# Performance work log

Hardware: AMD Instinct MI355X
Metric: run time of the kernel (lower is better)

The kernel has to match this reference:

```python
import jax, jax.numpy as jnp
import numpy as np
from jax import lax

CLIP = 5.0
LN_EPS = 1e-5


def _embed(feats, mean, std, W, b, g, beta):
    # InputNorm (eval mode, count>1): normalize with running stats, clamp.
    h = jnp.clip((feats - mean) / std, -CLIP, CLIP)
    h = lax.stop_gradient(h)  # torch runs InputNorm under no_grad
    # Linear + ReLU
    h = jax.nn.relu(h @ W + b)
    # LayerNorm over d_model
    mu = h.mean(-1, keepdims=True)
    var = ((h - mu) ** 2).mean(-1, keepdims=True)
    return (h - mu) / jnp.sqrt(var + LN_EPS) * g + beta


def setup_inputs() -> dict:
    key = jax.random.key(0)
    ks = jax.random.split(key, 8)
    nA, fA = 300000, 32
    nB, fB = 150000, 48
    d = 256
    B = 512
    inp = {
        "featsA": jax.random.normal(ks[0], (nA, fA), jnp.float32),
        "featsB": jax.random.normal(ks[1], (nB, fB), jnp.float32),
        "normA_mean": jnp.zeros((fA,), jnp.float32),
        "normA_std": jnp.ones((fA,), jnp.float32),
        "normB_mean": jnp.zeros((fB,), jnp.float32),
        "normB_std": jnp.ones((fB,), jnp.float32),
        "WA": jax.random.normal(ks[2], (fA, d), jnp.float32) / np.sqrt(fA),
        "bA": jnp.zeros((d,), jnp.float32),
        "lnA_g": jnp.ones((d,), jnp.float32),
        "lnA_b": jnp.zeros((d,), jnp.float32),
        "WB_": jax.random.normal(ks[3], (fB, d), jnp.float32) / np.sqrt(fB),
        "bB": jnp.zeros((d,), jnp.float32),
        "lnB_g": jnp.ones((d,), jnp.float32),
        "lnB_b": jnp.zeros((d,), jnp.float32),
        "Wback": jax.random.normal(ks[4], (d, d), jnp.float32) / np.sqrt(d),
        "bback": jnp.zeros((d,), jnp.float32),
        "Wv": jax.random.normal(ks[5], (d, 1), jnp.float32) / np.sqrt(d),
        "bv": jnp.zeros((1,), jnp.float32),
        "batch_index": jax.random.randint(ks[6], (nA + nB,), 0, B, jnp.int64)
        if jax.config.jax_enable_x64 else jax.random.randint(ks[6], (nA + nB,), 0, B, jnp.int32).astype(jnp.int32),
        "num_obs": B,
    }
    return inp


def reference(featsA, featsB, normA_mean, normA_std, normB_mean, normB_std,
              WA, bA, lnA_g, lnA_b, WB_, bB, lnB_g, lnB_b,
              Wback, bback, Wv, bv, batch_index, num_obs):
    # Per-entity-type embedding stacks, concatenated in entity-type order
    xA = _embed(featsA, normA_mean, normA_std, WA, bA, lnA_g, lnA_b)
    xB = _embed(featsB, normB_mean, normB_std, WB_, bB, lnB_g, lnB_b)
    x = jnp.concatenate([xA, xB], axis=0)          # [N, d]
    x = jax.nn.relu(x @ Wback + bback)              # backbone
    # torch_scatter mean pooling over observations
    sums = jax.ops.segment_sum(x, batch_index, num_segments=num_obs)
    counts = jax.ops.segment_sum(jnp.ones((x.shape[0],), x.dtype), batch_index,
                                 num_segments=num_obs)
    pooled = sums / jnp.maximum(counts, 1.0)[:, None]  # empty segments -> 0
    return pooled @ Wv + bv                          # [num_obs, 1]
```

## Files before the change

kernel.cpp:

```cpp
#include <hip/hip_runtime.h>

#define NSEG 512
#define NSPLIT 32

typedef __attribute__((ext_vector_type(8))) short short8;
typedef __attribute__((ext_vector_type(4))) short short4v;
typedef __attribute__((ext_vector_type(4))) float floatx4;

#define WS_WAT   0
#define WS_WBT2  16384
#define WS_W2GA  49152
#define WS_W2GB  180224
#define WS_C1A   311296
#define WS_C2A   312320
#define WS_C1B   313344
#define WS_C2B   314368
#define WS_INVA  315392
#define WS_INVB  315520
#define WS_VPART 315712
#define WS_CPART 381248

__device__ __forceinline__ short f2bf(float f) {
  unsigned u = __builtin_bit_cast(unsigned, f);
  u += 0x7FFFu + ((u >> 16) & 1u);
  return (short)(u >> 16);
}

__global__ void prep_kernel(const float* __restrict__ WA, const float* __restrict__ WB,
                            const float* __restrict__ Wback,
                            const float* __restrict__ gA, const float* __restrict__ betaA,
                            const float* __restrict__ gB, const float* __restrict__ betaB,
                            const float* __restrict__ bback,
                            const float* __restrict__ sA, const float* __restrict__ sB,
                            char* __restrict__ ws) {
  short* waT  = (short*)(ws + WS_WAT);
  short* wbT2 = (short*)(ws + WS_WBT2);
  short* w2gA = (short*)(ws + WS_W2GA);
  short* w2gB = (short*)(ws + WS_W2GB);
  float* c1A = (float*)(ws + WS_C1A);
  float* c2A = (float*)(ws + WS_C2A);
  float* c1B = (float*)(ws + WS_C1B);
  float* c2B = (float*)(ws + WS_C2B);
  float* invA = (float*)(ws + WS_INVA);
  float* invB = (float*)(ws + WS_INVB);
  float* vz   = (float*)(ws + WS_VPART);
  int tid = blockIdx.x * blockDim.x + threadIdx.x;
  int stride = gridDim.x * blockDim.x;
  for (int i = tid; i < 32*256; i += stride) {
    int n = i >> 5, k = i & 31;
    waT[i] = f2bf(WA[k*256 + n]);
  }
  for (int i = tid; i < 256*64; i += stride) {
    int n = i >> 6, k = i & 63;
    wbT2[i] = (k < 48) ? f2bf(WB[k*256 + n]) : (short)0;
  }
  for (int i = tid; i < 256*256; i += stride) {
    int n = i >> 8, k = i & 255;
    float w = Wback[k*256 + n];
    w2gA[i] = f2bf(gA[k] * w);
    w2gB[i] = f2bf(gB[k] * w);
  }
  if (blockIdx.x < 4 && threadIdx.x < 256) {
    int n = threadIdx.x;
    int which = blockIdx.x;
    const float* coef = (which == 0) ? gA : (which == 1) ? betaA : (which == 2) ? gB : betaB;
    float a = 0.f;
    #pragma unroll 8
    for (int k = 0; k < 256; k++) a = fmaf(coef[k], Wback[k*256 + n], a);
    if (which == 0)      c1A[n] = a;
    else if (which == 1) c2A[n] = a + bback[n];
    else if (which == 2) c1B[n] = a;
    else                 c2B[n] = a + bback[n];
  }
  if (tid < 32) invA[tid] = 1.0f / sA[tid];
  if (tid < 48) invB[tid] = 1.0f / sB[tid];
  for (int i = tid; i < 2*NSPLIT*NSEG; i += stride) vz[i] = 0.0f;
}

__global__ __launch_bounds__(256, 4) void fused_kernel(
    const float* __restrict__ featsA, const float* __restrict__ featsB,
    const float* __restrict__ mA, const float* __restrict__ mB,
    const float* __restrict__ bA, const float* __restrict__ bB,
    const float* __restrict__ Wv, const int* __restrict__ bidx,
    const char* __restrict__ ws, float* __restrict__ vpart, float* __restrict__ cpart,
    int tilesA, int nA, int nB)
{
  __shared__ __attribute__((aligned(16))) short ztile[64*264];
  __shared__ __attribute__((aligned(16))) float sred[64][4];
  __shared__ __attribute__((aligned(16))) float s2red[64][4];
  __shared__ __attribute__((aligned(16))) float vpw[64][4];

  const int tid  = threadIdx.x;
  const int wave = tid >> 6;
  const int lane = tid & 63;
  const int l15  = lane & 15;
  const int quad = lane >> 4;

  const bool isA = (blockIdx.x < (unsigned)tilesA);
  const int  tb  = isA ? blockIdx.x : (blockIdx.x - tilesA);
  const int  r0  = tb * 64;
  const int  nrows = isA ? nA : nB;
  const int  valid = min(64, nrows - r0);
  const float* feats = isA ? featsA : featsB;
  const float* meanp = isA ? mA : mB;
  const float* invp  = (const float*)(ws + (isA ? WS_INVA : WS_INVB));
  const float* biasp = isA ? bA : bB;
  const short* weT   = (const short*)(ws + (isA ? WS_WAT : WS_WBT2));
  const short* w2gT  = (const short*)(ws + (isA ? WS_W2GA : WS_W2GB));
  const float* c1p   = (const float*)(ws + (isA ? WS_C1A : WS_C1B));
  const float* c2p   = (const float*)(ws + (isA ? WS_C2A : WS_C2B));
  const int f       = isA ? 32 : 48;
  const int kstride = isA ? 32 : 64;
  const int ksteps  = isA ? 1 : 2;

  floatx4 acc1[4][4];
  #pragma unroll
  for (int mt = 0; mt < 4; mt++)
    #pragma unroll
    for (int nt = 0; nt < 4; nt++)
      acc1[mt][nt] = 0.0f;

  for (int kk = 0; kk < ksteps; kk++) {
    const int k0 = kk*32 + quad*8;
    const bool kvalid = (k0 < f);
    floatx4 mv0 = {0,0,0,0}, mv1 = {0,0,0,0}, iv0 = {1,1,1,1}, iv1 = {1,1,1,1};
    if (kvalid) {
      mv0 = *(const floatx4*)(meanp + k0);  mv1 = *(const floatx4*)(meanp + k0 + 4);
      iv0 = *(const floatx4*)(invp + k0);   iv1 = *(const floatx4*)(invp + k0 + 4);
    }
    short8 bfw[4];
    #pragma unroll
    for (int nt = 0; nt < 4; nt++)
      bfw[nt] = *(const short8*)(weT + (size_t)(64*wave + 16*nt + l15) * kstride + kk*32 + quad*8);
    #pragma unroll
    for (int mt = 0; mt < 4; mt++) {
      short8 a = {0,0,0,0,0,0,0,0};
      int row = 16*mt + l15;
      if (kvalid && row < valid) {
        const float* fp = feats + (size_t)(r0 + row) * f + k0;
        floatx4 x0 = *(const floatx4*)fp;
        floatx4 x1 = *(const floatx4*)(fp + 4);
        #pragma unroll
        for (int e = 0; e < 4; e++) {
          float h0 = (x0[e] - mv0[e]) * iv0[e];
          h0 = fminf(fmaxf(h0, -5.0f), 5.0f);
          a[e] = f2bf(h0);
          float h1 = (x1[e] - mv1[e]) * iv1[e];
          h1 = fminf(fmaxf(h1, -5.0f), 5.0f);
          a[4+e] = f2bf(h1);
        }
      }
      #pragma unroll
      for (int nt = 0; nt < 4; nt++)
        acc1[mt][nt] = __builtin_amdgcn_mfma_f32_16x16x32_bf16(bfw[nt], a, acc1[mt][nt], 0, 0, 0);
    }
  }

  float sacc[4], s2acc[4];
  #pragma unroll
  for (int mt = 0; mt < 4; mt++) { sacc[mt] = 0.f; s2acc[mt] = 0.f; }

  #pragma unroll
  for (int nt = 0; nt < 4; nt++) {
    const int c0 = 64*wave + 16*nt + 4*quad;
    floatx4 b1v = *(const floatx4*)(biasp + c0);
    #pragma unroll
    for (int mt = 0; mt < 4; mt++) {
      short4v pk;
      #pragma unroll
      for (int r = 0; r < 4; r++) {
        float h = fmaxf(acc1[mt][nt][r] + b1v[r], 0.0f);
        sacc[mt] += h;
        s2acc[mt] = fmaf(h, h, s2acc[mt]);
        pk[r] = f2bf(h);
      }
      *(short4v*)(ztile + (16*mt + l15)*264 + c0) = pk;
    }
  }
  #pragma unroll
  for (int mt = 0; mt < 4; mt++) {
    float s = sacc[mt], s2 = s2acc[mt];
    s += __shfl_xor(s, 16, 64);  s2 += __shfl_xor(s2, 16, 64);
    s += __shfl_xor(s, 32, 64);  s2 += __shfl_xor(s2, 32, 64);
    if (lane < 16) {
      sred[16*mt + lane][wave] = s;
      s2red[16*mt + lane][wave] = s2;
    }
  }
  __syncthreads();

  float rsv[4], mrsv[4];
  #pragma unroll
  for (int mt = 0; mt < 4; mt++) {
    int row = 16*mt + l15;
    floatx4 sv  = *(const floatx4*)sred[row];
    floatx4 s2v = *(const floatx4*)s2red[row];
    float s  = sv[0] + sv[1] + sv[2] + sv[3];
    float s2 = s2v[0] + s2v[1] + s2v[2] + s2v[3];
    float mu  = s * (1.0f/256.0f);
    float var = fmaxf(s2 * (1.0f/256.0f) - mu*mu, 0.0f);
    float rs  = rsqrtf(var + 1e-5f);
    rsv[mt]  = rs;
    mrsv[mt] = mu * rs;
  }

  floatx4 acc2[4][4];
  #pragma unroll
  for (int mt = 0; mt < 4; mt++)
    #pragma unroll
    for (int nt = 0; nt < 4; nt++)
      acc2[mt][nt] = 0.0f;

  #pragma unroll 2
  for (int kk = 0; kk < 8; kk++) {
    short8 bf[4];
    #pragma unroll
    for (int nt = 0; nt < 4; nt++)
      bf[nt] = *(const short8*)(w2gT + (size_t)(64*wave + 16*nt + l15)*256 + kk*32 + quad*8);
    #pragma unroll
    for (int mt = 0; mt < 4; mt++) {
      short8 a = *(const short8*)(ztile + (16*mt + l15)*264 + kk*32 + quad*8);
      #pragma unroll
      for (int nt = 0; nt < 4; nt++)
        acc2[mt][nt] = __builtin_amdgcn_mfma_f32_16x16x32_bf16(bf[nt], a, acc2[mt][nt], 0, 0, 0);
    }
  }

  float pv[4] = {0.f, 0.f, 0.f, 0.f};
  #pragma unroll
  for (int nt = 0; nt < 4; nt++) {
    const int c0 = 64*wave + 16*nt + 4*quad;
    floatx4 c1v = *(const floatx4*)(c1p + c0);
    floatx4 c2v = *(const floatx4*)(c2p + c0);
    floatx4 wvv = *(const floatx4*)(Wv + c0);
    #pragma unroll
    for (int mt = 0; mt < 4; mt++) {
      float rs = rsv[mt], mrs = mrsv[mt];
      #pragma unroll
      for (int r = 0; r < 4; r++) {
        float t = fmaf(-mrs, c1v[r], c2v[r]);
        float y = fmaf(rs, acc2[mt][nt][r], t);
        y = fmaxf(y, 0.0f);
        pv[mt] = fmaf(y, wvv[r], pv[mt]);
      }
    }
  }
  #pragma unroll
  for (int mt = 0; mt < 4; mt++) {
    float p = pv[mt];
    p += __shfl_xor(p, 16, 64);
    p += __shfl_xor(p, 32, 64);
    if (lane < 16) vpw[16*mt + lane][wave] = p;
  }
  __syncthreads();

  if (tid < valid) {
    floatx4 vv = *(const floatx4*)vpw[tid];
    float v = vv[0] + vv[1] + vv[2] + vv[3];
    int g = (isA ? r0 : (nA + r0)) + tid;
    int seg = bidx[g];
    int split = blockIdx.x & (NSPLIT - 1);
    atomicAdd(&vpart[split*NSEG + seg], v);
    atomicAdd(&cpart[split*NSEG + seg], 1.0f);
  }
}

__global__ void final_kernel(const float* __restrict__ vpart, const float* __restrict__ cpart,
                             const float* __restrict__ bv, float* __restrict__ out, int nseg) {
  int s = blockIdx.x * blockDim.x + threadIdx.x;
  if (s < nseg) {
    float a = 0.0f, c = 0.0f;
    #pragma unroll 8
    for (int i = 0; i < NSPLIT; i++) { a += vpart[i*NSEG + s]; c += cpart[i*NSEG + s]; }
    out[s] = a / fmaxf(c, 1.0f) + bv[0];
  }
}

extern "C" void kernel_launch(void* const* d_in, const int* in_sizes, int n_in,
                              void* d_out, int out_size, void* d_ws, size_t ws_size,
                              hipStream_t stream) {
  const float* featsA = (const float*)d_in[0];
  const float* featsB = (const float*)d_in[1];
  const float* mA     = (const float*)d_in[2];
  const float* sA     = (const float*)d_in[3];
  const float* mB     = (const float*)d_in[4];
  const float* sB     = (const float*)d_in[5];
  const float* WA     = (const float*)d_in[6];
  const float* bA     = (const float*)d_in[7];
  const float* gA     = (const float*)d_in[8];
  const float* betaA  = (const float*)d_in[9];
  const float* WB     = (const float*)d_in[10];
  const float* bB     = (const float*)d_in[11];
  const float* gB     = (const float*)d_in[12];
  const float* betaB  = (const float*)d_in[13];
  const float* Wback  = (const float*)d_in[14];
  const float* bback  = (const float*)d_in[15];
  const float* Wv     = (const float*)d_in[16];
  const float* bv     = (const float*)d_in[17];
  const int*   bidx   = (const int*)d_in[18];

  const int nA = in_sizes[0] / 32;
  const int nB = in_sizes[1] / 48;
  char* ws = (char*)d_ws;
  float* vpart = (float*)(ws + WS_VPART);
  float* cpart = (float*)(ws + WS_CPART);
  float* out = (float*)d_out;

  prep_kernel<<<256, 256, 0, stream>>>(WA, WB, Wback, gA, betaA, gB, betaB,
                                       bback, sA, sB, ws);

  const int tilesA = (nA + 63) / 64;
  const int tilesB = (nB + 63) / 64;
  fused_kernel<<<tilesA + tilesB, 256, 0, stream>>>(
      featsA, featsB, mA, mB, bA, bB, Wv, bidx, ws, vpart, cpart, tilesA, nA, nB);

  final_kernel<<<(out_size + 255) / 256, 256, 0, stream>>>(vpart, cpart, bv, out, out_size);
}
```

Baseline: 307.3 us.

## Use packed bf16 conversions, pad LDS stride, relax launch bounds, reorder GEMM2

Replaces the manual per-element bf16 rounding with packed bf16x2 conversions, and widens the LDS tile row stride from 264 to 276 to change the bank mapping. It lowers the launch-bounds occupancy hint from 4 to 3 blocks per CU, which gives the compiler more registers. It also moves the second GEMM ahead of the LayerNorm statistics computation and hoists the weight loads in the first GEMM. Several small changes are bundled here; the lower occupancy could reduce latency hiding, and the 276 stride may break 16-byte alignment of the LDS vector reads.

```diff
diff --git a/kernel.cpp b/kernel.cpp
--- a/kernel.cpp
+++ b/kernel.cpp
@@ -1,11 +1,14 @@
 #include <hip/hip_runtime.h>
+#include <hip/hip_bf16.h>
 
 #define NSEG 512
 #define NSPLIT 32
+#define ZSTR 276
 
 typedef __attribute__((ext_vector_type(8))) short short8;
-typedef __attribute__((ext_vector_type(4))) short short4v;
 typedef __attribute__((ext_vector_type(4))) float floatx4;
+typedef __attribute__((ext_vector_type(4))) unsigned uintx4;
+typedef __attribute__((ext_vector_type(2))) unsigned uintx2;
 
 #define WS_WAT   0
 #define WS_WBT2  16384
@@ -26,26 +29,32 @@
   return (short)(u >> 16);
 }
 
-__global__ void prep_kernel(const float* __restrict__ WA, const float* __restrict__ WB,
-                            const float* __restrict__ Wback,
-                            const float* __restrict__ gA, const float* __restrict__ betaA,
-                            const float* __restrict__ gB, const float* __restrict__ betaB,
-                            const float* __restrict__ bback,
-                            const float* __restrict__ sA, const float* __restrict__ sB,
-                            char* __restrict__ ws) {
+__device__ __forceinline__ unsigned cvt2(float lo, float hi) {
+  __hip_bfloat162 b = __float22bfloat162_rn(float2{lo, hi});
+  unsigned r;
+  __builtin_memcpy(&r, &b, 4);
+  return r;
+}
+
+__global__ __launch_bounds__(256) void prep_kernel(
+    const float* __restrict__ WA, const float* __restrict__ WB,
+    const float* __restrict__ Wback,
+    const float* __restrict__ gA, const float* __restrict__ betaA,
+    const float* __restrict__ gB, const float* __restrict__ betaB,
+    const float* __restrict__ bback,
+    const float* __restrict__ sA, const float* __restrict__ sB,
+    char* __restrict__ ws) {
   short* waT  = (short*)(ws + WS_WAT);
   short* wbT2 = (short*)(ws + WS_WBT2);
   short* w2gA = (short*)(ws + WS_W2GA);
   short* w2gB = (short*)(ws + WS_W2GB);
-  float* c1A = (float*)(ws + WS_C1A);
-  float* c2A = (float*)(ws + WS_C2A);
-  float* c1B = (float*)(ws + WS_C1B);
-  float* c2B = (float*)(ws + WS_C2B);
   float* invA = (float*)(ws + WS_INVA);
   float* invB = (float*)(ws + WS_INVB);
   float* vz   = (float*)(ws + WS_VPART);
   int tid = blockIdx.x * blockDim.x + threadIdx.x;
   int stride = gridDim.x * blockDim.x;
+  if (tid < 32) invA[tid] = 1.0f / sA[tid];
+  if (tid < 48) invB[tid] = 1.0f / sB[tid];
   for (int i = tid; i < 32*256; i += stride) {
     int n = i >> 5, k = i & 31;
     waT[i] = f2bf(WA[k*256 + n]);
@@ -60,24 +69,21 @@
     w2gA[i] = f2bf(gA[k] * w);
     w2gB[i] = f2bf(gB[k] * w);
   }
-  if (blockIdx.x < 4 && threadIdx.x < 256) {
+  if (blockIdx.x < 4) {
     int n = threadIdx.x;
     int which = blockIdx.x;
     const float* coef = (which == 0) ? gA : (which == 1) ? betaA : (which == 2) ? gB : betaB;
     float a = 0.f;
     #pragma unroll 8
     for (int k = 0; k < 256; k++) a = fmaf(coef[k], Wback[k*256 + n], a);
-    if (which == 0)      c1A[n] = a;
-    else if (which == 1) c2A[n] = a + bback[n];
-    else if (which == 2) c1B[n] = a;
-    else                 c2B[n] = a + bback[n];
-  }
-  if (tid < 32) invA[tid] = 1.0f / sA[tid];
-  if (tid < 48) invB[tid] = 1.0f / sB[tid];
+    float* dst = (float*)(ws + ((which == 0) ? WS_C1A : (which == 1) ? WS_C2A
+                               : (which == 2) ? WS_C1B : WS_C2B));
+    dst[n] = a + ((which & 1) ? bback[n] : 0.0f);
+  }
   for (int i = tid; i < 2*NSPLIT*NSEG; i += stride) vz[i] = 0.0f;
 }
 
-__global__ __launch_bounds__(256, 4) void fused_kernel(
+__global__ __launch_bounds__(256, 3) void fused_kernel(
     const float* __restrict__ featsA, const float* __restrict__ featsB,
     const float* __restrict__ mA, const float* __restrict__ mB,
     const float* __restrict__ bA, const float* __restrict__ bB,
@@ -85,7 +91,7 @@
     const char* __restrict__ ws, float* __restrict__ vpart, float* __restrict__ cpart,
     int tilesA, int nA, int nB)
 {
-  __shared__ __attribute__((aligned(16))) short ztile[64*264];
+  __shared__ __attribute__((aligned(16))) short ztile[64*ZSTR];
   __shared__ __attribute__((aligned(16))) float sred[64][4];
   __shared__ __attribute__((aligned(16))) float s2red[64][4];
   __shared__ __attribute__((aligned(16))) float vpw[64][4];
@@ -101,6 +107,8 @@
   const int  r0  = tb * 64;
   const int  nrows = isA ? nA : nB;
   const int  valid = min(64, nrows - r0);
+  const int  gbase = (isA ? r0 : (nA + r0));
+  const int  split = blockIdx.x & (NSPLIT - 1);
   const float* feats = isA ? featsA : featsB;
   const float* meanp = isA ? mA : mB;
   const float* invp  = (const float*)(ws + (isA ? WS_INVA : WS_INVB));
@@ -121,6 +129,12 @@
       acc1[mt][nt] = 0.0f;
 
   for (int kk = 0; kk < ksteps; kk++) {
+    short8 bfw[4];
+    #pragma unroll
+    for (int nt = 0; nt < 4; nt++) {
+      unsigned boff = (unsigned)(64*wave + 16*nt + l15) * kstride + kk*32 + quad*8;
+      bfw[nt] = *(const short8*)(weT + boff);
+    }
     const int k0 = kk*32 + quad*8;
     const bool kvalid = (k0 < f);
     floatx4 mv0 = {0,0,0,0}, mv1 = {0,0,0,0}, iv0 = {1,1,1,1}, iv1 = {1,1,1,1};
@@ -128,10 +142,6 @@
       mv0 = *(const floatx4*)(meanp + k0);  mv1 = *(const floatx4*)(meanp + k0 + 4);
       iv0 = *(const floatx4*)(invp + k0);   iv1 = *(const floatx4*)(invp + k0 + 4);
     }
-    short8 bfw[4];
-    #pragma unroll
-    for (int nt = 0; nt < 4; nt++)
-      bfw[nt] = *(const short8*)(weT + (size_t)(64*wave + 16*nt + l15) * kstride + kk*32 + quad*8);
     #pragma unroll
     for (int mt = 0; mt < 4; mt++) {
       short8 a = {0,0,0,0,0,0,0,0};
@@ -140,15 +150,16 @@
         const float* fp = feats + (size_t)(r0 + row) * f + k0;
         floatx4 x0 = *(const floatx4*)fp;
         floatx4 x1 = *(const floatx4*)(fp + 4);
-        #pragma unroll
-        for (int e = 0; e < 4; e++) {
-          float h0 = (x0[e] - mv0[e]) * iv0[e];
-          h0 = fminf(fmaxf(h0, -5.0f), 5.0f);
-          a[e] = f2bf(h0);
-          float h1 = (x1[e] - mv1[e]) * iv1[e];
-          h1 = fminf(fmaxf(h1, -5.0f), 5.0f);
-          a[4+e] = f2bf(h1);
-        }
+        float g0 = fminf(fmaxf((x0[0] - mv0[0]) * iv0[0], -5.0f), 5.0f);
+        float g1 = fminf(fmaxf((x0[1] - mv0[1]) * iv0[1], -5.0f), 5.0f);
+        float g2 = fminf(fmaxf((x0[2] - mv0[2]) * iv0[2], -5.0f), 5.0f);
+        float g3 = fminf(fmaxf((x0[3] - mv0[3]) * iv0[3], -5.0f), 5.0f);
+        float g4 = fminf(fmaxf((x1[0] - mv1[0]) * iv1[0], -5.0f), 5.0f);
+        float g5 = fminf(fmaxf((x1[1] - mv1[1]) * iv1[1], -5.0f), 5.0f);
+        float g6 = fminf(fmaxf((x1[2] - mv1[2]) * iv1[2], -5.0f), 5.0f);
+        float g7 = fminf(fmaxf((x1[3] - mv1[3]) * iv1[3], -5.0f), 5.0f);
+        uintx4 u = { cvt2(g0, g1), cvt2(g2, g3), cvt2(g4, g5), cvt2(g6, g7) };
+        a = __builtin_bit_cast(short8, u);
       }
       #pragma unroll
       for (int nt = 0; nt < 4; nt++)
@@ -156,25 +167,21 @@
     }
   }
 
-  float sacc[4], s2acc[4];
-  #pragma unroll
-  for (int mt = 0; mt < 4; mt++) { sacc[mt] = 0.f; s2acc[mt] = 0.f; }
-
+  float sacc[4] = {0.f,0.f,0.f,0.f}, s2acc[4] = {0.f,0.f,0.f,0.f};
   #pragma unroll
   for (int nt = 0; nt < 4; nt++) {
     const int c0 = 64*wave + 16*nt + 4*quad;
     floatx4 b1v = *(const floatx4*)(biasp + c0);
     #pragma unroll
     for (int mt = 0; mt < 4; mt++) {
-      short4v pk;
-      #pragma unroll
-      for (int r = 0; r < 4; r++) {
-        float h = fmaxf(acc1[mt][nt][r] + b1v[r], 0.0f);
-        sacc[mt] += h;
-        s2acc[mt] = fmaf(h, h, s2acc[mt]);
-        pk[r] = f2bf(h);
-      }
-      *(short4v*)(ztile + (16*mt + l15)*264 + c0) = pk;
+      float h0 = fmaxf(acc1[mt][nt][0] + b1v[0], 0.0f);
+      float h1 = fmaxf(acc1[mt][nt][1] + b1v[1], 0.0f);
+      float h2 = fmaxf(acc1[mt][nt][2] + b1v[2], 0.0f);
+      float h3 = fmaxf(acc1[mt][nt][3] + b1v[3], 0.0f);
+      sacc[mt] += (h0 + h1) + (h2 + h3);
+      s2acc[mt] = fmaf(h0, h0, fmaf(h1, h1, fmaf(h2, h2, fmaf(h3, h3, s2acc[mt]))));
+      uintx2 pk = { cvt2(h0, h1), cvt2(h2, h3) };
+      *(uintx2*)(ztile + (16*mt + l15)*ZSTR + c0) = pk;
     }
   }
   #pragma unroll
@@ -188,6 +195,30 @@
     }
   }
   __syncthreads();
+
+  floatx4 acc2[4][4];
+  #pragma unroll
+  for (int mt = 0; mt < 4; mt++)
+    #pragma unroll
+    for (int nt = 0; nt < 4; nt++)
+      acc2[mt][nt] = 0.0f;
+
+  #pragma unroll 2
+  for (int kk = 0; kk < 8; kk++) {
+    short8 bf[4];
+    #pragma unroll
+    for (int nt = 0; nt < 4; nt++) {
+      unsigned goff = (unsigned)(64*wave + 16*nt + l15)*256 + kk*32 + quad*8;
+      bf[nt] = *(const short8*)(w2gT + goff);
+    }
+    #pragma unroll
+    for (int mt = 0; mt < 4; mt++) {
+      short8 a = *(const short8*)(ztile + (16*mt + l15)*ZSTR + kk*32 + quad*8);
+      #pragma unroll
+      for (int nt = 0; nt < 4; nt++)
+        acc2[mt][nt] = __builtin_amdgcn_mfma_f32_16x16x32_bf16(bf[nt], a, acc2[mt][nt], 0, 0, 0);
+    }
+  }
 
   float rsv[4], mrsv[4];
   #pragma unroll
@@ -204,28 +235,6 @@
     mrsv[mt] = mu * rs;
   }
 
-  floatx4 acc2[4][4];
-  #pragma unroll
-  for (int mt = 0; mt < 4; mt++)
-    #pragma unroll
-    for (int nt = 0; nt < 4; nt++)
-      acc2[mt][nt] = 0.0f;
-
-  #pragma unroll 2
-  for (int kk = 0; kk < 8; kk++) {
-    short8 bf[4];
-    #pragma unroll
-    for (int nt = 0; nt < 4; nt++)
-      bf[nt] = *(const short8*)(w2gT + (size_t)(64*wave + 16*nt + l15)*256 + kk*32 + quad*8);
-    #pragma unroll
-    for (int mt = 0; mt < 4; mt++) {
-      short8 a = *(const short8*)(ztile + (16*mt + l15)*264 + kk*32 + quad*8);
-      #pragma unroll
-      for (int nt = 0; nt < 4; nt++)
-        acc2[mt][nt] = __builtin_amdgcn_mfma_f32_16x16x32_bf16(bf[nt], a, acc2[mt][nt], 0, 0, 0);
-    }
-  }
-
   float pv[4] = {0.f, 0.f, 0.f, 0.f};
   #pragma unroll
   for (int nt = 0; nt < 4; nt++) {
@@ -257,9 +266,7 @@
   if (tid < valid) {
     floatx4 vv = *(const floatx4*)vpw[tid];
     float v = vv[0] + vv[1] + vv[2] + vv[3];
-    int g = (isA ? r0 : (nA + r0)) + tid;
-    int seg = bidx[g];
-    int split = blockIdx.x & (NSPLIT - 1);
+    int seg = bidx[gbase + tid];
     atomicAdd(&vpart[split*NSEG + seg], v);
     atomicAdd(&cpart[split*NSEG + seg], 1.0f);
   }
@@ -314,5 +321,6 @@
   fused_kernel<<<tilesA + tilesB, 256, 0, stream>>>(
       featsA, featsB, mA, mB, bA, bB, Wv, bidx, ws, vpart, cpart, tilesA, nA, nB);
 
-  final_kernel<<<(out_size + 255) / 256, 256, 0, stream>>>(vpart, cpart, bv, out, out_size);
-}
+  if (out_size > 0)
+    final_kernel<<<(out_size + 255) / 256, 256, 0, stream>>>(vpart, cpart, bv, out, out_size);
+}
```

After: 296.8 us. 3.4% less time.
